# Kernel tuning notes

Hardware: AMD Instinct MI355X
Metric: run time of the kernel (lower is better)

## Reference

```python
import jax, jax.numpy as jnp
import numpy as np

T, H, E, I, K, G, KG = 16384, 1024, 64, 768, 8, 8, 4


def setup_inputs() -> dict:
    key = jax.random.key(0)
    ks = jax.random.split(key, 6)
    return {
        "hidden_states": jax.random.normal(ks[0], (T, H), jnp.float32),
        "gate_weight": jax.random.normal(ks[1], (E, H), jnp.float32) * 0.02,
        "correction_bias": jax.random.normal(ks[2], (E,), jnp.float32) * 0.01,
        "w_gate": jax.random.normal(ks[3], (E, I, H), jnp.float32) * 0.02,
        "w_up": jax.random.normal(ks[4], (E, I, H), jnp.float32) * 0.02,
        "w_down": jax.random.normal(ks[5], (E, H, I), jnp.float32) * 0.02,
    }


def _grouped_topk(hidden, gate_w, bias, top_k=K, n_group=G, topk_group=KG, renormalize=True):
    # gate runs in fp32 (MoEGate.dtype = float32)
    logits = hidden.astype(jnp.float32) @ gate_w.T  # [T, E]
    scores = jax.nn.sigmoid(logits)  # noaux_tc uses sigmoid scores
    s_choice = scores + bias[None, :].astype(jnp.float32)
    t, e = scores.shape
    # group score = sum of top-2 biased scores within each group
    grouped = s_choice.reshape(t, n_group, e // n_group)
    top2, _ = jax.lax.top_k(grouped, 2)
    group_scores = top2.sum(-1)  # [T, G]
    _, gidx = jax.lax.top_k(group_scores, topk_group)  # [T, KG]
    gmask = jnp.zeros((t, n_group), jnp.float32).at[jnp.arange(t)[:, None], gidx].set(1.0)
    emask = jnp.repeat(gmask, e // n_group, axis=1)  # [T, E]
    masked = jnp.where(emask > 0, s_choice, -jnp.inf)
    _, topk_idx = jax.lax.top_k(masked, top_k)  # [T, K]
    # weights use the unbiased sigmoid scores
    topk_w = jnp.take_along_axis(scores, topk_idx, axis=1)
    if renormalize:
        topk_w = topk_w / (topk_w.sum(-1, keepdims=True) + 1e-20)
    # routed_scaling_factor = 1.0
    return topk_idx, topk_w


def reference(hidden_states, gate_weight, correction_bias, w_gate, w_up, w_down):
    t = hidden_states.shape[0]
    topk_idx, topk_w = _grouped_topk(hidden_states, gate_weight, correction_bias)
    # dense combine weights [T, E]: zero except at selected experts
    combine = jnp.zeros((t, E), hidden_states.dtype).at[
        jnp.arange(t)[:, None], topk_idx
    ].add(topk_w.astype(hidden_states.dtype))

    def step(acc, xs):
        wg, wu, wd, c = xs  # wg/wu: [I,H], wd: [H,I], c: [T]
        h = jax.nn.silu(hidden_states @ wg.T) * (hidden_states @ wu.T)  # [T, I]
        return acc + c[:, None] * (h @ wd.T), None

    acc0 = jnp.zeros_like(hidden_states)
    out, _ = jax.lax.scan(step, acc0, (w_gate, w_up, w_down, combine.T))
    return out
```

## Files before the change

### kernel.cpp

```cpp
#include <hip/hip_runtime.h>
#include <hip/hip_bf16.h>
#include <math.h>

#define T_TOK 16384
#define H_DIM 1024
#define E_NUM 64
#define I_DIM 768
#define TOPK  8
#define NGRP  8
#define KGRP  4
#define S_ASN (T_TOK*TOPK)
#define BM 128
#define BK 64
#define MAXBLK (S_ASN/BM + E_NUM)

typedef __attribute__((ext_vector_type(4))) float f4v;
typedef __attribute__((ext_vector_type(8))) short s8v;

#define GLDS16(g, l) __builtin_amdgcn_global_load_lds( \
    (const __attribute__((address_space(1))) void*)(g), \
    (__attribute__((address_space(3))) void*)(l), 16, 0, 0)

static __device__ __forceinline__ short f2bf(float f){
  union { float f; unsigned u; } a; a.f = f;
  unsigned u = a.u;
  unsigned r = (u + 0x7fffu + ((u >> 16) & 1u)) >> 16;
  return (short)r;
}
static __device__ __forceinline__ s8v cvt8(f4v a, f4v b){
  s8v r;
  r[0]=f2bf(a[0]); r[1]=f2bf(a[1]); r[2]=f2bf(a[2]); r[3]=f2bf(a[3]);
  r[4]=f2bf(b[0]); r[5]=f2bf(b[1]); r[6]=f2bf(b[2]); r[7]=f2bf(b[3]);
  return r;
}

__launch_bounds__(256)
__global__ void cast_kernel(const float* __restrict__ src,
                            short* __restrict__ dst, long n8)
{
  long i = (long)blockIdx.x*blockDim.x + threadIdx.x;
  long stride = (long)gridDim.x*blockDim.x;
  for (; i < n8; i += stride){
    f4v a = *(const f4v*)(src + i*8);
    f4v b = *(const f4v*)(src + i*8 + 4);
    *(s8v*)(dst + i*8) = cvt8(a, b);
  }
}

__launch_bounds__(256)
__global__ void gate_kernel(const float* __restrict__ hidden,
                            const float* __restrict__ gate_w,
                            double* __restrict__ logits)
{
  __shared__ float sX[64][33];
  __shared__ float sW[64][33];
  const int tid  = threadIdx.x;
  const int t0   = blockIdx.x * 64;
  const int srow = tid >> 2;
  const int scol = (tid & 3) * 8;
  const int tx = tid & 15, ty = tid >> 4;
  double acc[4][4];
  #pragma unroll
  for (int i=0;i<4;i++)
    #pragma unroll
    for (int j=0;j<4;j++) acc[i][j]=0.0;

  for (int k0=0;k0<H_DIM;k0+=32){
    f4v a0 = *(const f4v*)&hidden[(size_t)(t0+srow)*H_DIM + k0 + scol];
    f4v a1 = *(const f4v*)&hidden[(size_t)(t0+srow)*H_DIM + k0 + scol + 4];
    f4v b0 = *(const f4v*)&gate_w[(size_t)srow*H_DIM + k0 + scol];
    f4v b1 = *(const f4v*)&gate_w[(size_t)srow*H_DIM + k0 + scol + 4];
    __syncthreads();
    #pragma unroll
    for (int j=0;j<4;j++){
      sX[srow][scol+j]   = a0[j];  sX[srow][scol+4+j] = a1[j];
      sW[srow][scol+j]   = b0[j];  sW[srow][scol+4+j] = b1[j];
    }
    __syncthreads();
    #pragma unroll
    for (int kk=0;kk<32;kk++){
      float xv[4], wv[4];
      #pragma unroll
      for (int i=0;i<4;i++){ xv[i]=sX[ty*4+i][kk]; wv[i]=sW[tx*4+i][kk]; }
      #pragma unroll
      for (int i=0;i<4;i++)
        #pragma unroll
        for (int j=0;j<4;j++)
          acc[i][j] += (double)xv[i] * (double)wv[j];
    }
  }
  #pragma unroll
  for (int i=0;i<4;i++)
    #pragma unroll
    for (int j=0;j<4;j++)
      logits[(size_t)(t0+ty*4+i)*E_NUM + tx*4+j] = acc[i][j];
}

__global__ void route_kernel(const double* __restrict__ logits,
                             const float*  __restrict__ bias,
                             int*   __restrict__ topk_idx,
                             float* __restrict__ topk_w,
                             int*   __restrict__ counts)
{
  const int t = blockIdx.x * blockDim.x + threadIdx.x;
  if (t >= T_TOK) return;
  const double* lg = logits + (size_t)t * E_NUM;
  double sc[E_NUM], sch[E_NUM];
  for (int e2=0;e2<E_NUM;e2++){
    double s = 1.0 / (1.0 + exp(-lg[e2]));
    sc[e2]  = s;
    sch[e2] = s + (double)bias[e2];
  }
  double gs[NGRP];
  for (int g=0;g<NGRP;g++){
    double m1=-1e300, m2=-1e300;
    for (int j=0;j<8;j++){
      double v = sch[g*8+j];
      if (v > m1){ m2 = m1; m1 = v; } else if (v > m2){ m2 = v; }
    }
    gs[g] = m1 + m2;
  }
  unsigned gsel = 0;
  for (int r=0;r<KGRP;r++){
    int best = 0; double bv = -1.0e308;
    for (int g=0;g<NGRP;g++)
      if (!((gsel>>g)&1u) && gs[g] > bv){ bv = gs[g]; best = g; }
    gsel |= 1u << best;
  }
  unsigned long long used = 0ULL;
  double wsum = 0.0;
  int sel[TOPK]; double w[TOPK];
  for (int r=0;r<TOPK;r++){
    int best = 0; double bv = -1.0e308;
    for (int e2=0;e2<E_NUM;e2++){
      if ((used>>e2)&1ULL) continue;
      if (!((gsel>>(e2>>3))&1u)) continue;
      if (sch[e2] > bv){ bv = sch[e2]; best = e2; }
    }
    used |= 1ULL << best;
    sel[r] = best;
    w[r]   = sc[best];
    wsum  += w[r];
  }
  double inv = 1.0 / (wsum + 1e-20);
  for (int r=0;r<TOPK;r++){
    topk_idx[(size_t)t*TOPK + r] = sel[r];
    topk_w  [(size_t)t*TOPK + r] = (float)(w[r]*inv);
    atomicAdd(&counts[sel[r]], 1);
  }
}

__global__ void scan_kernel(const int* __restrict__ counts,
                            int* __restrict__ offsets,
                            int* __restrict__ blk_start)
{
  if (threadIdx.x == 0 && blockIdx.x == 0){
    int off = 0, blk = 0;
    for (int e=0;e<E_NUM;e++){
      offsets[e] = off; blk_start[e] = blk;
      off += counts[e];
      blk += (counts[e] + BM - 1) / BM;
    }
    offsets[E_NUM] = off; blk_start[E_NUM] = blk;
  }
}

__global__ void scatter_kernel(const int* __restrict__ topk_idx,
                               const float* __restrict__ topk_w,
                               const int* __restrict__ offsets,
                               int* __restrict__ cursor,
                               int* __restrict__ token_list,
                               float* __restrict__ weight_list)
{
  const int t = blockIdx.x*blockDim.x + threadIdx.x;
  if (t >= T_TOK) return;
  for (int r=0;r<TOPK;r++){
    int   e2 = topk_idx[(size_t)t*TOPK + r];
    float wv = topk_w [(size_t)t*TOPK + r];
    int p = atomicAdd(&cursor[e2], 1);
    token_list [offsets[e2] + p] = t;
    weight_list[offsets[e2] + p] = wv;
  }
}


__launch_bounds__(256, 3)
__global__ void ffn1_fast(const short* __restrict__ hid_bf,
                          const short* __restrict__ wg_bf,
                          const short* __restrict__ wu_bf,
                          const int*   __restrict__ token_list,
                          const float* __restrict__ weight_list,
                          const int*   __restrict__ offsets,
                          const int*   __restrict__ blk_start,
                          short*       __restrict__ h_all)
{
  __shared__ short lsX[128*64];
  __shared__ short lsG[64*64];
  __shared__ short lsU[64*64];
  __shared__ float lsWt[128];

  const int bx = blockIdx.x;
  if (bx >= blk_start[E_NUM]) return;
  int e = 0;
  while (blk_start[e+1] <= bx) ++e;
  const int rb   = bx - blk_start[e];
  const int cb   = blockIdx.y;
  const int base = offsets[e];
  const int n_e  = offsets[e+1] - base;
  const int row0 = rb * BM;

  const int tid = threadIdx.x;
  const int lane = tid & 63, wid = tid >> 6;
  const int wm = wid >> 1, wn = wid & 1;
  const int l15 = lane & 15, l4 = lane >> 4;

  if (tid < BM) lsWt[tid] = ((row0+tid) < n_e) ? weight_list[base+row0+tid] : 0.f;

  const short* srcA[4];
  #pragma unroll
  for (int i=0;i<4;i++){
    int s_lin = i*256 + tid;
    int row = s_lin >> 3, sl = s_lin & 7;
    int asn = base + row0 + row; if (asn >= S_ASN) asn = S_ASN-1;
    int tok = token_list[asn];
    srcA[i] = hid_bf + (size_t)tok*H_DIM + ((sl ^ (row&7))<<3);
  }
  const short* srcG[2]; const short* srcU[2];
  #pragma unroll
  for (int i=0;i<2;i++){
    int s_lin = i*256 + tid;
    int row = s_lin >> 3, sl = s_lin & 7;
    size_t wrow = ((size_t)e*I_DIM + cb*64 + row)*H_DIM + ((sl ^ (row&7))<<3);
    srcG[i] = wg_bf + wrow;
    srcU[i] = wu_bf + wrow;
  }
  short* dstA0 = lsX + wid*512;
  short* dstG0 = lsG + wid*512;
  short* dstU0 = lsU + wid*512;

  f4v accg[4][2], accu[4][2];
  #pragma unroll
  for (int m=0;m<4;m++)
    #pragma unroll
    for (int n=0;n<2;n++){
      accg[m][n]=(f4v){0.f,0.f,0.f,0.f};
      accu[m][n]=(f4v){0.f,0.f,0.f,0.f};
    }

  for (int k0=0; k0<H_DIM; k0+=BK){
    __syncthreads();
    #pragma unroll
    for (int i=0;i<4;i++) GLDS16(srcA[i]+k0, dstA0 + i*2048);
    #pragma unroll
    for (int i=0;i<2;i++) GLDS16(srcG[i]+k0, dstG0 + i*2048);
    #pragma unroll
    for (int i=0;i<2;i++) GLDS16(srcU[i]+k0, dstU0 + i*2048);
    __syncthreads();
    #pragma unroll
    for (int kk=0;kk<2;kk++){
      s8v af[4], bg[2], bu[2];
      #pragma unroll
      for (int m=0;m<4;m++){
        int r = wm*64 + m*16 + l15;
        int s = (kk*4 + l4) ^ (r & 7);
        af[m] = *(const s8v*)&lsX[r*64 + (s<<3)];
      }
      #pragma unroll
      for (int n=0;n<2;n++){
        int r = wn*32 + n*16 + l15;
        int s = (kk*4 + l4) ^ (r & 7);
        bg[n] = *(const s8v*)&lsG[r*64 + (s<<3)];
        bu[n] = *(const s8v*)&lsU[r*64 + (s<<3)];
      }
      #pragma unroll
      for (int m=0;m<4;m++)
        #pragma unroll
        for (int n=0;n<2;n++){
          accg[m][n] = __builtin_amdgcn_mfma_f32_16x16x32_bf16(af[m], bg[n], accg[m][n], 0,0,0);
          accu[m][n] = __builtin_amdgcn_mfma_f32_16x16x32_bf16(af[m], bu[n], accu[m][n], 0,0,0);
        }
    }
  }
  #pragma unroll
  for (int m=0;m<4;m++){
    #pragma unroll
    for (int i=0;i<4;i++){
      int r = wm*64 + m*16 + l4*4 + i;
      if (row0 + r < n_e){
        float wgt = lsWt[r];
        size_t hb = (size_t)(base+row0+r)*I_DIM + (size_t)cb*64;
        #pragma unroll
        for (int n=0;n<2;n++){
          int c = wn*32 + n*16 + l15;
          float g = accg[m][n][i], u = accu[m][n][i];
          float s = g / (1.f + __expf(-g));
          h_all[hb + c] = f2bf(s * u * wgt);
        }
      }
    }
  }
}

__launch_bounds__(256, 3)
__global__ void ffn2_fast(const short* __restrict__ h_all,
                          const short* __restrict__ wd_bf,
                          const int*   __restrict__ token_list,
                          const int*   __restrict__ offsets,
                          const int*   __restrict__ blk_start,
                          float*       __restrict__ out)
{
  __shared__ short lsA[128*64];
  __shared__ short lsB[128*64];
  __shared__ int   lsT[128];

  const int bx = blockIdx.x;
  if (bx >= blk_start[E_NUM]) return;
  int e = 0;
  while (blk_start[e+1] <= bx) ++e;
  const int rb   = bx - blk_start[e];
  const int cb   = blockIdx.y;
  const int base = offsets[e];
  const int n_e  = offsets[e+1] - base;
  const int row0 = rb * BM;

  const int tid = threadIdx.x;
  const int lane = tid & 63, wid = tid >> 6;
  const int wm = wid >> 1, wn = wid & 1;
  const int l15 = lane & 15, l4 = lane >> 4;

  if (tid < BM) lsT[tid] = ((row0+tid) < n_e) ? token_list[base+row0+tid] : -1;

  const short* srcA[4]; const short* srcB[4];
  #pragma unroll
  for (int i=0;i<4;i++){
    int s_lin = i*256 + tid;
    int row = s_lin >> 3, sl = s_lin & 7;
    int arow = base + row0 + row; if (arow >= S_ASN) arow = S_ASN-1;
    srcA[i] = h_all + (size_t)arow*I_DIM + ((sl ^ (row&7))<<3);
    srcB[i] = wd_bf + ((size_t)e*H_DIM + cb*128 + row)*I_DIM + ((sl ^ (row&7))<<3);
  }
  short* dstA0 = lsA + wid*512;
  short* dstB0 = lsB + wid*512;

  f4v acc[4][4];
  #pragma unroll
  for (int m=0;m<4;m++)
    #pragma unroll
    for (int n=0;n<4;n++) acc[m][n]=(f4v){0.f,0.f,0.f,0.f};

  for (int k0=0; k0<I_DIM; k0+=BK){
    __syncthreads();
    #pragma unroll
    for (int i=0;i<4;i++) GLDS16(srcA[i]+k0, dstA0 + i*2048);
    #pragma unroll
    for (int i=0;i<4;i++) GLDS16(srcB[i]+k0, dstB0 + i*2048);
    __syncthreads();
    #pragma unroll
    for (int kk=0;kk<2;kk++){
      s8v af[4], bf[4];
      #pragma unroll
      for (int m=0;m<4;m++){
        int r = wm*64 + m*16 + l15;
        int s = (kk*4 + l4) ^ (r & 7);
        af[m] = *(const s8v*)&lsA[r*64 + (s<<3)];
      }
      #pragma unroll
      for (int n=0;n<4;n++){
        int r = wn*64 + n*16 + l15;
        int s = (kk*4 + l4) ^ (r & 7);
        bf[n] = *(const s8v*)&lsB[r*64 + (s<<3)];
      }
      #pragma unroll
      for (int m=0;m<4;m++)
        #pragma unroll
        for (int n=0;n<4;n++)
          acc[m][n] = __builtin_amdgcn_mfma_f32_16x16x32_bf16(af[m], bf[n], acc[m][n], 0,0,0);
    }
  }
  #pragma unroll
  for (int m=0;m<4;m++){
    #pragma unroll
    for (int i=0;i<4;i++){
      int r = wm*64 + m*16 + l4*4 + i;
      int tk = lsT[r];
      if (tk >= 0){
        #pragma unroll
        for (int n=0;n<4;n++){
          int c = cb*128 + wn*64 + n*16 + l15;
          atomicAdd(&out[(size_t)tk*H_DIM + c], acc[m][n][i]);
        }
      }
    }
  }
}

__launch_bounds__(512, 2)
__global__ void ffn1_kernel(const float* __restrict__ hidden,
                            const float* __restrict__ w_gate,
                            const float* __restrict__ w_up,
                            const int*   __restrict__ token_list,
                            const float* __restrict__ weight_list,
                            const int*   __restrict__ offsets,
                            const int*   __restrict__ blk_start,
                            short*       __restrict__ h_all)
{
  __shared__ short lsX[BM*64];
  __shared__ short lsG[BM*64];
  __shared__ short lsU[BM*64];
  __shared__ float lsWt[BM];

  const int bx = blockIdx.x;
  if (bx >= blk_start[E_NUM]) return;
  int e = 0;
  while (blk_start[e+1] <= bx) ++e;
  const int rb   = bx - blk_start[e];
  const int cb   = blockIdx.y;
  const int base = offsets[e];
  const int n_e  = offsets[e+1] - base;
  const int row0 = rb * BM;

  const int tid   = threadIdx.x;
  const int srow  = tid >> 2;
  const int scol  = (tid & 3) << 4;
  const int slot0 = (tid & 3) << 1;
  const int wsl0  = srow*64 + (((slot0  ) ^ (srow & 7)) << 3);
  const int wsl1  = srow*64 + (((slot0+1) ^ (srow & 7)) << 3);

  const bool tvalid = (row0 + srow) < n_e;
  int tok = 0;
  if (tvalid) tok = token_list[base + row0 + srow];
  const float* xsrc = hidden + (size_t)tok * H_DIM + scol;
  const size_t woff = (size_t)e * I_DIM * H_DIM + (size_t)(cb*128 + srow) * H_DIM + scol;
  const float* gsrc = w_gate + woff;
  const float* usrc = w_up   + woff;

  const int lane = tid & 63, wid = tid >> 6;
  const int wm = wid >> 2, wn = wid & 3;
  const int l15 = lane & 15, l4 = lane >> 4;

  f4v accg[4][2], accu[4][2];
  #pragma unroll
  for (int m=0;m<4;m++)
    #pragma unroll
    for (int n=0;n<2;n++){
      accg[m][n]=(f4v){0.f,0.f,0.f,0.f};
      accu[m][n]=(f4v){0.f,0.f,0.f,0.f};
    }

  for (int k0=0; k0<H_DIM; k0+=BK){
    f4v x0,x1,x2,x3;
    if (tvalid){
      x0 = *(const f4v*)(xsrc+k0);   x1 = *(const f4v*)(xsrc+k0+4);
      x2 = *(const f4v*)(xsrc+k0+8); x3 = *(const f4v*)(xsrc+k0+12);
    } else {
      x0=x1=x2=x3=(f4v){0.f,0.f,0.f,0.f};
    }
    f4v g0 = *(const f4v*)(gsrc+k0),   g1 = *(const f4v*)(gsrc+k0+4);
    f4v g2 = *(const f4v*)(gsrc+k0+8), g3 = *(const f4v*)(gsrc+k0+12);
    f4v u0 = *(const f4v*)(usrc+k0),   u1 = *(const f4v*)(usrc+k0+4);
    f4v u2 = *(const f4v*)(usrc+k0+8), u3 = *(const f4v*)(usrc+k0+12);
    __syncthreads();
    *(s8v*)&lsX[wsl0] = cvt8(x0,x1);  *(s8v*)&lsX[wsl1] = cvt8(x2,x3);
    *(s8v*)&lsG[wsl0] = cvt8(g0,g1);  *(s8v*)&lsG[wsl1] = cvt8(g2,g3);
    *(s8v*)&lsU[wsl0] = cvt8(u0,u1);  *(s8v*)&lsU[wsl1] = cvt8(u2,u3);
    __syncthreads();
    #pragma unroll
    for (int kk=0;kk<2;kk++){
      s8v af[4], bg[2], bu[2];
      #pragma unroll
      for (int m=0;m<4;m++){
        int r = wm*64 + m*16 + l15;
        int s = (kk*4 + l4) ^ (r & 7);
        af[m] = *(const s8v*)&lsX[r*64 + (s<<3)];
      }
      #pragma unroll
      for (int n=0;n<2;n++){
        int r = wn*32 + n*16 + l15;
        int s = (kk*4 + l4) ^ (r & 7);
        bg[n] = *(const s8v*)&lsG[r*64 + (s<<3)];
        bu[n] = *(const s8v*)&lsU[r*64 + (s<<3)];
      }
      #pragma unroll
      for (int m=0;m<4;m++)
        #pragma unroll
        for (int n=0;n<2;n++){
          accg[m][n] = __builtin_amdgcn_mfma_f32_16x16x32_bf16(af[m], bg[n], accg[m][n], 0,0,0);
          accu[m][n] = __builtin_amdgcn_mfma_f32_16x16x32_bf16(af[m], bu[n], accu[m][n], 0,0,0);
        }
    }
  }
  if (tid < BM) lsWt[tid] = ((row0+tid) < n_e) ? weight_list[base+row0+tid] : 0.f;
  __syncthreads();
  #pragma unroll
  for (int m=0;m<4;m++){
    #pragma unroll
    for (int i=0;i<4;i++){
      int r = wm*64 + m*16 + l4*4 + i;
      if (row0 + r < n_e){
        float wgt = lsWt[r];
        size_t hb = (size_t)(base+row0+r)*I_DIM + (size_t)cb*128;
        #pragma unroll
        for (int n=0;n<2;n++){
          int c = wn*32 + n*16 + l15;
          float g = accg[m][n][i], u = accu[m][n][i];
          float s = g / (1.f + __expf(-g));
          h_all[hb + c] = f2bf(s * u * wgt);
        }
      }
    }
  }
}

__launch_bounds__(512, 2)
__global__ void ffn2_kernel(const short* __restrict__ h_all,
                            const float* __restrict__ w_down,
                            const int*   __restrict__ token_list,
                            const int*   __restrict__ offsets,
                            const int*   __restrict__ blk_start,
                            float*       __restrict__ out)
{
  __shared__ short lsA[BM*64];
  __shared__ short lsB[BM*64];
  __shared__ int   lsT[BM];

  const int bx = blockIdx.x;
  if (bx >= blk_start[E_NUM]) return;
  int e = 0;
  while (blk_start[e+1] <= bx) ++e;
  const int rb   = bx - blk_start[e];
  const int cb   = blockIdx.y;
  const int base = offsets[e];
  const int n_e  = offsets[e+1] - base;
  const int row0 = rb * BM;

  const int tid   = threadIdx.x;
  const int srow  = tid >> 2;
  const int slot0 = (tid & 3) << 1;
  const int wsl0  = srow*64 + (((slot0  ) ^ (srow & 7)) << 3);
  const int wsl1  = srow*64 + (((slot0+1) ^ (srow & 7)) << 3);

  int arow = base + row0 + srow;
  if (arow >= S_ASN) arow = S_ASN - 1;
  const short* asrc = h_all + (size_t)arow*I_DIM + ((tid&3)<<4);
  const float* bsrc = w_down + (size_t)e*H_DIM*I_DIM
                    + (size_t)(cb*128 + srow)*I_DIM + ((tid&3)<<4);

  const int lane = tid & 63, wid = tid >> 6;
  const int wm = wid >> 2, wn = wid & 3;
  const int l15 = lane & 15, l4 = lane >> 4;

  f4v acc[4][2];
  #pragma unroll
  for (int m=0;m<4;m++)
    #pragma unroll
    for (int n=0;n<2;n++) acc[m][n]=(f4v){0.f,0.f,0.f,0.f};

  for (int k0=0; k0<I_DIM; k0+=BK){
    s8v alo = *(const s8v*)(asrc + k0);
    s8v ahi = *(const s8v*)(asrc + k0 + 8);
    f4v b0 = *(const f4v*)(bsrc+k0),   b1 = *(const f4v*)(bsrc+k0+4);
    f4v b2 = *(const f4v*)(bsrc+k0+8), b3 = *(const f4v*)(bsrc+k0+12);
    __syncthreads();
    *(s8v*)&lsA[wsl0] = alo;          *(s8v*)&lsA[wsl1] = ahi;
    *(s8v*)&lsB[wsl0] = cvt8(b0,b1);  *(s8v*)&lsB[wsl1] = cvt8(b2,b3);
    __syncthreads();
    #pragma unroll
    for (int kk=0;kk<2;kk++){
      s8v af[4], bf[2];
      #pragma unroll
      for (int m=0;m<4;m++){
        int r = wm*64 + m*16 + l15;
        int s = (kk*4 + l4) ^ (r & 7);
        af[m] = *(const s8v*)&lsA[r*64 + (s<<3)];
      }
      #pragma unroll
      for (int n=0;n<2;n++){
        int r = wn*32 + n*16 + l15;
        int s = (kk*4 + l4) ^ (r & 7);
        bf[n] = *(const s8v*)&lsB[r*64 + (s<<3)];
      }
      #pragma unroll
      for (int m=0;m<4;m++)
        #pragma unroll
        for (int n=0;n<2;n++)
          acc[m][n] = __builtin_amdgcn_mfma_f32_16x16x32_bf16(af[m], bf[n], acc[m][n], 0,0,0);
    }
  }
  if (tid < BM) lsT[tid] = ((row0+tid) < n_e) ? token_list[base+row0+tid] : -1;
  __syncthreads();
  #pragma unroll
  for (int m=0;m<4;m++){
    #pragma unroll
    for (int i=0;i<4;i++){
      int r = wm*64 + m*16 + l4*4 + i;
      int tk = lsT[r];
      if (tk >= 0){
        #pragma unroll
        for (int n=0;n<2;n++){
          int c = cb*128 + wn*32 + n*16 + l15;
          atomicAdd(&out[(size_t)tk*H_DIM + c], acc[m][n][i]);
        }
      }
    }
  }
}

extern "C" void kernel_launch(void* const* d_in, const int* in_sizes, int n_in,
                              void* d_out, int out_size, void* d_ws, size_t ws_size,
                              hipStream_t stream)
{
  const float* hidden = (const float*)d_in[0];
  const float* gate_w = (const float*)d_in[1];
  const float* bias   = (const float*)d_in[2];
  const float* w_gate = (const float*)d_in[3];
  const float* w_up   = (const float*)d_in[4];
  const float* w_down = (const float*)d_in[5];
  float* out = (float*)d_out;

  char* ws = (char*)d_ws;
  size_t off = 0;
  #define WALLOC(bytes) (ws + off); off += (((size_t)(bytes)) + 255) & ~(size_t)255
  double* logits    = (double*)WALLOC((size_t)T_TOK*E_NUM*8);
  int*    topk_idx  = (int*)   WALLOC((size_t)T_TOK*TOPK*4);
  float*  topk_w    = (float*) WALLOC((size_t)T_TOK*TOPK*4);
  int*    counts    = (int*)   WALLOC(256);
  int*    cursor    = (int*)   WALLOC(256);
  int*    offsets   = (int*)   WALLOC(512);
  int*    blk_st    = (int*)   WALLOC(512);
  int*    token_l   = (int*)   WALLOC((size_t)S_ASN*4);
  float*  weight_l  = (float*) WALLOC((size_t)S_ASN*4);
  short*  h_all     = (short*) WALLOC((size_t)S_ASN*I_DIM*2);
  const size_t base_need = off;
  short*  hid_bf    = (short*) WALLOC((size_t)T_TOK*H_DIM*2);
  short*  wg_bf     = (short*) WALLOC((size_t)E_NUM*I_DIM*H_DIM*2);
  short*  wu_bf     = (short*) WALLOC((size_t)E_NUM*I_DIM*H_DIM*2);
  short*  wd_bf     = (short*) WALLOC((size_t)E_NUM*H_DIM*I_DIM*2);
  const size_t fast_need = off;
  #undef WALLOC

  const bool fast = (ws_size >= fast_need);
  if (ws_size < base_need) return;

  hipMemsetAsync(counts, 0, 512, stream);
  hipMemsetAsync(out, 0, (size_t)T_TOK*H_DIM*4, stream);

  gate_kernel   <<<T_TOK/64,  256, 0, stream>>>(hidden, gate_w, logits);
  route_kernel  <<<T_TOK/256, 256, 0, stream>>>(logits, bias, topk_idx, topk_w, counts);
  scan_kernel   <<<1, 64, 0, stream>>>(counts, offsets, blk_st);
  scatter_kernel<<<T_TOK/256, 256, 0, stream>>>(topk_idx, topk_w, offsets, cursor,
                                                token_l, weight_l);
  if (fast){
    long n8h = (long)T_TOK*H_DIM/8;
    long n8w = (long)E_NUM*I_DIM*H_DIM/8;
    cast_kernel<<<2048, 256, 0, stream>>>(hidden, hid_bf, n8h);
    cast_kernel<<<2048, 256, 0, stream>>>(w_gate, wg_bf, n8w);
    cast_kernel<<<2048, 256, 0, stream>>>(w_up,   wu_bf, n8w);
    cast_kernel<<<2048, 256, 0, stream>>>(w_down, wd_bf, n8w);
    dim3 g1(MAXBLK, I_DIM/64);
    ffn1_fast<<<g1, 256, 0, stream>>>(hid_bf, wg_bf, wu_bf, token_l, weight_l,
                                      offsets, blk_st, h_all);
    dim3 g2(MAXBLK, H_DIM/128);
    ffn2_fast<<<g2, 256, 0, stream>>>(h_all, wd_bf, token_l, offsets, blk_st, out);
  } else {
    dim3 g1(MAXBLK, I_DIM/128);
    ffn1_kernel<<<g1, 512, 0, stream>>>(hidden, w_gate, w_up, token_l, weight_l,
                                        offsets, blk_st, h_all);
    dim3 g2(MAXBLK, H_DIM/128);
    ffn2_kernel<<<g2, 512, 0, stream>>>(h_all, w_down, token_l, offsets, blk_st, out);
  }
}
```

Baseline: 1.923 ms.

## Pin experts to XCDs with per-XCD work tables and grid-stride tile loops

Builds per-XCD work tables in which each expert's tiles all go to one XCD (expert e maps to XCD e&7), filled by a new fill_kernel from offsets computed in the scan. The FFN kernels now launch a fixed grid and stride over their XCD's table, so the blocks that share an expert's weights run on the same XCD and reuse them through its L2. The aim is to cut repeated weight fetches from HBM. Launch bounds also go from 3 to 4 blocks per CU. The risks are load imbalance across XCDs when expert counts are uneven, and the assumption that blocks are dealt to XCDs round-robin by blockIdx.

```diff
diff --git a/kernel.cpp b/kernel.cpp
--- a/kernel.cpp
+++ b/kernel.cpp
@@ -13,6 +13,10 @@
 #define BM 128
 #define BK 64
 #define MAXBLK (S_ASN/BM + E_NUM)
+#define NCB1 (I_DIM/64)
+#define NCB2 (H_DIM/128)
+#define XCAP 16384
+#define XSTRIDE 2048
 
 typedef __attribute__((ext_vector_type(4))) float f4v;
 typedef __attribute__((ext_vector_type(8))) short s8v;
@@ -152,17 +156,42 @@
 
 __global__ void scan_kernel(const int* __restrict__ counts,
                             int* __restrict__ offsets,
-                            int* __restrict__ blk_start)
+                            int* __restrict__ blk_start,
+                            int* __restrict__ xoff,
+                            int* __restrict__ qblk)
 {
   if (threadIdx.x == 0 && blockIdx.x == 0){
     int off = 0, blk = 0;
+    int cnt[8];
+    for (int x=0;x<8;x++) cnt[x]=0;
     for (int e=0;e<E_NUM;e++){
       offsets[e] = off; blk_start[e] = blk;
+      int nblk = (counts[e] + BM - 1) / BM;
+      xoff[e] = cnt[e & 7];
+      cnt[e & 7] += nblk;
       off += counts[e];
-      blk += (counts[e] + BM - 1) / BM;
+      blk += nblk;
     }
     offsets[E_NUM] = off; blk_start[E_NUM] = blk;
-  }
+    for (int x=0;x<8;x++) qblk[x] = cnt[x];
+  }
+}
+
+__global__ void fill_kernel(const int* __restrict__ offsets,
+                            const int* __restrict__ xoff,
+                            int* __restrict__ tab1,
+                            int* __restrict__ tab2)
+{
+  const int e = blockIdx.x;
+  const int n_e  = offsets[e+1] - offsets[e];
+  const int nblk = (n_e + BM - 1) / BM;
+  const int x = e & 7;
+  int* t1 = tab1 + (size_t)x*XCAP + xoff[e]*NCB1;
+  int* t2 = tab2 + (size_t)x*XCAP + xoff[e]*NCB2;
+  for (int i = threadIdx.x; i < nblk*NCB1; i += blockDim.x)
+    t1[i] = (e<<18) | ((i/NCB1)<<4) | (i%NCB1);
+  for (int i = threadIdx.x; i < nblk*NCB2; i += blockDim.x)
+    t2[i] = (e<<18) | ((i/NCB2)<<4) | (i%NCB2);
 }
 
 __global__ void scatter_kernel(const int* __restrict__ topk_idx,
@@ -184,14 +213,15 @@
 }
 
 
-__launch_bounds__(256, 3)
+__launch_bounds__(256, 4)
 __global__ void ffn1_fast(const short* __restrict__ hid_bf,
                           const short* __restrict__ wg_bf,
                           const short* __restrict__ wu_bf,
                           const int*   __restrict__ token_list,
                           const float* __restrict__ weight_list,
                           const int*   __restrict__ offsets,
-                          const int*   __restrict__ blk_start,
+                          const int*   __restrict__ tab1,
+                          const int*   __restrict__ qblk,
                           short*       __restrict__ h_all)
 {
   __shared__ short lsX[128*64];
@@ -199,195 +229,204 @@
   __shared__ short lsU[64*64];
   __shared__ float lsWt[128];
 
-  const int bx = blockIdx.x;
-  if (bx >= blk_start[E_NUM]) return;
-  int e = 0;
-  while (blk_start[e+1] <= bx) ++e;
-  const int rb   = bx - blk_start[e];
-  const int cb   = blockIdx.y;
-  const int base = offsets[e];
-  const int n_e  = offsets[e+1] - base;
-  const int row0 = rb * BM;
-
+  const int xcd = blockIdx.x & 7;
+  const int q0  = blockIdx.x >> 3;
+  const int qn  = qblk[xcd] * NCB1;
   const int tid = threadIdx.x;
   const int lane = tid & 63, wid = tid >> 6;
   const int wm = wid >> 1, wn = wid & 1;
   const int l15 = lane & 15, l4 = lane >> 4;
 
-  if (tid < BM) lsWt[tid] = ((row0+tid) < n_e) ? weight_list[base+row0+tid] : 0.f;
-
-  const short* srcA[4];
-  #pragma unroll
-  for (int i=0;i<4;i++){
-    int s_lin = i*256 + tid;
-    int row = s_lin >> 3, sl = s_lin & 7;
-    int asn = base + row0 + row; if (asn >= S_ASN) asn = S_ASN-1;
-    int tok = token_list[asn];
-    srcA[i] = hid_bf + (size_t)tok*H_DIM + ((sl ^ (row&7))<<3);
-  }
-  const short* srcG[2]; const short* srcU[2];
-  #pragma unroll
-  for (int i=0;i<2;i++){
-    int s_lin = i*256 + tid;
-    int row = s_lin >> 3, sl = s_lin & 7;
-    size_t wrow = ((size_t)e*I_DIM + cb*64 + row)*H_DIM + ((sl ^ (row&7))<<3);
-    srcG[i] = wg_bf + wrow;
-    srcU[i] = wu_bf + wrow;
-  }
-  short* dstA0 = lsX + wid*512;
-  short* dstG0 = lsG + wid*512;
-  short* dstU0 = lsU + wid*512;
-
-  f4v accg[4][2], accu[4][2];
-  #pragma unroll
-  for (int m=0;m<4;m++)
-    #pragma unroll
-    for (int n=0;n<2;n++){
-      accg[m][n]=(f4v){0.f,0.f,0.f,0.f};
-      accu[m][n]=(f4v){0.f,0.f,0.f,0.f};
-    }
-
-  for (int k0=0; k0<H_DIM; k0+=BK){
+  for (int q = q0; q < qn; q += XSTRIDE){
+    const int v  = tab1[(size_t)xcd*XCAP + q];
+    const int e  = v >> 18;
+    const int rb = (v >> 4) & 16383;
+    const int cb = v & 15;
+    const int base = offsets[e];
+    const int n_e  = offsets[e+1] - base;
+    const int row0 = rb * BM;
+
     __syncthreads();
-    #pragma unroll
-    for (int i=0;i<4;i++) GLDS16(srcA[i]+k0, dstA0 + i*2048);
-    #pragma unroll
-    for (int i=0;i<2;i++) GLDS16(srcG[i]+k0, dstG0 + i*2048);
-    #pragma unroll
-    for (int i=0;i<2;i++) GLDS16(srcU[i]+k0, dstU0 + i*2048);
-    __syncthreads();
-    #pragma unroll
-    for (int kk=0;kk<2;kk++){
-      s8v af[4], bg[2], bu[2];
-      #pragma unroll
-      for (int m=0;m<4;m++){
-        int r = wm*64 + m*16 + l15;
-        int s = (kk*4 + l4) ^ (r & 7);
-        af[m] = *(const s8v*)&lsX[r*64 + (s<<3)];
-      }
+    if (tid < BM) lsWt[tid] = ((row0+tid) < n_e) ? weight_list[base+row0+tid] : 0.f;
+
+    const short* srcA[4];
+    #pragma unroll
+    for (int i=0;i<4;i++){
+      int s_lin = i*256 + tid;
+      int row = s_lin >> 3, sl = s_lin & 7;
+      int asn = base + row0 + row; if (asn >= S_ASN) asn = S_ASN-1;
+      int tok = token_list[asn];
+      srcA[i] = hid_bf + (size_t)tok*H_DIM + ((sl ^ (row&7))<<3);
+    }
+    const short* srcG[2]; const short* srcU[2];
+    #pragma unroll
+    for (int i=0;i<2;i++){
+      int s_lin = i*256 + tid;
+      int row = s_lin >> 3, sl = s_lin & 7;
+      size_t wrow = ((size_t)e*I_DIM + cb*64 + row)*H_DIM + ((sl ^ (row&7))<<3);
+      srcG[i] = wg_bf + wrow;
+      srcU[i] = wu_bf + wrow;
+    }
+    short* dstA0 = lsX + wid*512;
+    short* dstG0 = lsG + wid*512;
+    short* dstU0 = lsU + wid*512;
+
+    f4v accg[4][2], accu[4][2];
+    #pragma unroll
+    for (int m=0;m<4;m++)
       #pragma unroll
       for (int n=0;n<2;n++){
-        int r = wn*32 + n*16 + l15;
-        int s = (kk*4 + l4) ^ (r & 7);
-        bg[n] = *(const s8v*)&lsG[r*64 + (s<<3)];
-        bu[n] = *(const s8v*)&lsU[r*64 + (s<<3)];
-      }
-      #pragma unroll
-      for (int m=0;m<4;m++)
+        accg[m][n]=(f4v){0.f,0.f,0.f,0.f};
+        accu[m][n]=(f4v){0.f,0.f,0.f,0.f};
+      }
+
+    for (int k0=0; k0<H_DIM; k0+=BK){
+      __syncthreads();
+      #pragma unroll
+      for (int i=0;i<4;i++) GLDS16(srcA[i]+k0, dstA0 + i*2048);
+      #pragma unroll
+      for (int i=0;i<2;i++) GLDS16(srcG[i]+k0, dstG0 + i*2048);
+      #pragma unroll
+      for (int i=0;i<2;i++) GLDS16(srcU[i]+k0, dstU0 + i*2048);
+      __syncthreads();
+      #pragma unroll
+      for (int kk=0;kk<2;kk++){
+        s8v af[4], bg[2], bu[2];
+        #pragma unroll
+        for (int m=0;m<4;m++){
+          int r = wm*64 + m*16 + l15;
+          int s = (kk*4 + l4) ^ (r & 7);
+          af[m] = *(const s8v*)&lsX[r*64 + (s<<3)];
+        }
         #pragma unroll
         for (int n=0;n<2;n++){
-          accg[m][n] = __builtin_amdgcn_mfma_f32_16x16x32_bf16(af[m], bg[n], accg[m][n], 0,0,0);
-          accu[m][n] = __builtin_amdgcn_mfma_f32_16x16x32_bf16(af[m], bu[n], accu[m][n], 0,0,0);
-        }
-    }
-  }
-  #pragma unroll
-  for (int m=0;m<4;m++){
-    #pragma unroll
-    for (int i=0;i<4;i++){
-      int r = wm*64 + m*16 + l4*4 + i;
-      if (row0 + r < n_e){
-        float wgt = lsWt[r];
-        size_t hb = (size_t)(base+row0+r)*I_DIM + (size_t)cb*64;
-        #pragma unroll
-        for (int n=0;n<2;n++){
-          int c = wn*32 + n*16 + l15;
-          float g = accg[m][n][i], u = accu[m][n][i];
-          float s = g / (1.f + __expf(-g));
-          h_all[hb + c] = f2bf(s * u * wgt);
-        }
-      }
-    }
-  }
-}
-
-__launch_bounds__(256, 3)
+          int r = wn*32 + n*16 + l15;
+          int s = (kk*4 + l4) ^ (r & 7);
+          bg[n] = *(const s8v*)&lsG[r*64 + (s<<3)];
+          bu[n] = *(const s8v*)&lsU[r*64 + (s<<3)];
+        }
+        #pragma unroll
+        for (int m=0;m<4;m++)
+          #pragma unroll
+          for (int n=0;n<2;n++){
+            accg[m][n] = __builtin_amdgcn_mfma_f32_16x16x32_bf16(af[m], bg[n], accg[m][n], 0,0,0);
+            accu[m][n] = __builtin_amdgcn_mfma_f32_16x16x32_bf16(af[m], bu[n], accu[m][n], 0,0,0);
+          }
+      }
+    }
+    #pragma unroll
+    for (int m=0;m<4;m++){
+      #pragma unroll
+      for (int i=0;i<4;i++){
+        int r = wm*64 + m*16 + l4*4 + i;
+        if (row0 + r < n_e){
+          float wgt = lsWt[r];
+          size_t hb = (size_t)(base+row0+r)*I_DIM + (size_t)cb*64;
+          #pragma unroll
+          for (int n=0;n<2;n++){
+            int c = wn*32 + n*16 + l15;
+            float g = accg[m][n][i], u = accu[m][n][i];
+            float s = g / (1.f + __expf(-g));
+            h_all[hb + c] = f2bf(s * u * wgt);
+          }
+        }
+      }
+    }
+  }
+}
+
+__launch_bounds__(256, 4)
 __global__ void ffn2_fast(const short* __restrict__ h_all,
                           const short* __restrict__ wd_bf,
                           const int*   __restrict__ token_list,
                           const int*   __restrict__ offsets,
-                          const int*   __restrict__ blk_start,
+                          const int*   __restrict__ tab2,
+                          const int*   __restrict__ qblk,
                           float*       __restrict__ out)
 {
   __shared__ short lsA[128*64];
   __shared__ short lsB[128*64];
   __shared__ int   lsT[128];
 
-  const int bx = blockIdx.x;
-  if (bx >= blk_start[E_NUM]) return;
-  int e = 0;
-  while (blk_start[e+1] <= bx) ++e;
-  const int rb   = bx - blk_start[e];
-  const int cb   = blockIdx.y;
-  const int base = offsets[e];
-  const int n_e  = offsets[e+1] - base;
-  const int row0 = rb * BM;
-
+  const int xcd = blockIdx.x & 7;
+  const int q0  = blockIdx.x >> 3;
+  const int qn  = qblk[xcd] * NCB2;
   const int tid = threadIdx.x;
   const int lane = tid & 63, wid = tid >> 6;
   const int wm = wid >> 1, wn = wid & 1;
   const int l15 = lane & 15, l4 = lane >> 4;
 
-  if (tid < BM) lsT[tid] = ((row0+tid) < n_e) ? token_list[base+row0+tid] : -1;
-
-  const short* srcA[4]; const short* srcB[4];
-  #pragma unroll
-  for (int i=0;i<4;i++){
-    int s_lin = i*256 + tid;
-    int row = s_lin >> 3, sl = s_lin & 7;
-    int arow = base + row0 + row; if (arow >= S_ASN) arow = S_ASN-1;
-    srcA[i] = h_all + (size_t)arow*I_DIM + ((sl ^ (row&7))<<3);
-    srcB[i] = wd_bf + ((size_t)e*H_DIM + cb*128 + row)*I_DIM + ((sl ^ (row&7))<<3);
-  }
-  short* dstA0 = lsA + wid*512;
-  short* dstB0 = lsB + wid*512;
-
-  f4v acc[4][4];
-  #pragma unroll
-  for (int m=0;m<4;m++)
-    #pragma unroll
-    for (int n=0;n<4;n++) acc[m][n]=(f4v){0.f,0.f,0.f,0.f};
-
-  for (int k0=0; k0<I_DIM; k0+=BK){
+  for (int q = q0; q < qn; q += XSTRIDE){
+    const int v  = tab2[(size_t)xcd*XCAP + q];
+    const int e  = v >> 18;
+    const int rb = (v >> 4) & 16383;
+    const int cb = v & 15;
+    const int base = offsets[e];
+    const int n_e  = offsets[e+1] - base;
+    const int row0 = rb * BM;
+
     __syncthreads();
-    #pragma unroll
-    for (int i=0;i<4;i++) GLDS16(srcA[i]+k0, dstA0 + i*2048);
-    #pragma unroll
-    for (int i=0;i<4;i++) GLDS16(srcB[i]+k0, dstB0 + i*2048);
-    __syncthreads();
-    #pragma unroll
-    for (int kk=0;kk<2;kk++){
-      s8v af[4], bf[4];
-      #pragma unroll
-      for (int m=0;m<4;m++){
-        int r = wm*64 + m*16 + l15;
-        int s = (kk*4 + l4) ^ (r & 7);
-        af[m] = *(const s8v*)&lsA[r*64 + (s<<3)];
-      }
-      #pragma unroll
-      for (int n=0;n<4;n++){
-        int r = wn*64 + n*16 + l15;
-        int s = (kk*4 + l4) ^ (r & 7);
-        bf[n] = *(const s8v*)&lsB[r*64 + (s<<3)];
-      }
-      #pragma unroll
-      for (int m=0;m<4;m++)
-        #pragma unroll
-        for (int n=0;n<4;n++)
-          acc[m][n] = __builtin_amdgcn_mfma_f32_16x16x32_bf16(af[m], bf[n], acc[m][n], 0,0,0);
-    }
-  }
-  #pragma unroll
-  for (int m=0;m<4;m++){
+    if (tid < BM) lsT[tid] = ((row0+tid) < n_e) ? token_list[base+row0+tid] : -1;
+
+    const short* srcA[4]; const short* srcB[4];
     #pragma unroll
     for (int i=0;i<4;i++){
-      int r = wm*64 + m*16 + l4*4 + i;
-      int tk = lsT[r];
-      if (tk >= 0){
+      int s_lin = i*256 + tid;
+      int row = s_lin >> 3, sl = s_lin & 7;
+      int arow = base + row0 + row; if (arow >= S_ASN) arow = S_ASN-1;
+      srcA[i] = h_all + (size_t)arow*I_DIM + ((sl ^ (row&7))<<3);
+      srcB[i] = wd_bf + ((size_t)e*H_DIM + cb*128 + row)*I_DIM + ((sl ^ (row&7))<<3);
+    }
+    short* dstA0 = lsA + wid*512;
+    short* dstB0 = lsB + wid*512;
+
+    f4v acc[4][4];
+    #pragma unroll
+    for (int m=0;m<4;m++)
+      #pragma unroll
+      for (int n=0;n<4;n++) acc[m][n]=(f4v){0.f,0.f,0.f,0.f};
+
+    for (int k0=0; k0<I_DIM; k0+=BK){
+      __syncthreads();
+      #pragma unroll
+      for (int i=0;i<4;i++) GLDS16(srcA[i]+k0, dstA0 + i*2048);
+      #pragma unroll
+      for (int i=0;i<4;i++) GLDS16(srcB[i]+k0, dstB0 + i*2048);
+      __syncthreads();
+      #pragma unroll
+      for (int kk=0;kk<2;kk++){
+        s8v af[4], bf[4];
+        #pragma unroll
+        for (int m=0;m<4;m++){
+          int r = wm*64 + m*16 + l15;
+          int s = (kk*4 + l4) ^ (r & 7);
+          af[m] = *(const s8v*)&lsA[r*64 + (s<<3)];
+        }
         #pragma unroll
         for (int n=0;n<4;n++){
-          int c = cb*128 + wn*64 + n*16 + l15;
-          atomicAdd(&out[(size_t)tk*H_DIM + c], acc[m][n][i]);
+          int r = wn*64 + n*16 + l15;
+          int s = (kk*4 + l4) ^ (r & 7);
+          bf[n] = *(const s8v*)&lsB[r*64 + (s<<3)];
+        }
+        #pragma unroll
+        for (int m=0;m<4;m++)
+          #pragma unroll
+          for (int n=0;n<4;n++)
+            acc[m][n] = __builtin_amdgcn_mfma_f32_16x16x32_bf16(af[m], bf[n], acc[m][n], 0,0,0);
+      }
+    }
+    #pragma unroll
+    for (int m=0;m<4;m++){
+      #pragma unroll
+      for (int i=0;i<4;i++){
+        int r = wm*64 + m*16 + l4*4 + i;
+        int tk = lsT[r];
+        if (tk >= 0){
+          #pragma unroll
+          for (int n=0;n<4;n++){
+            int c = cb*128 + wn*64 + n*16 + l15;
+            atomicAdd(&out[(size_t)tk*H_DIM + c], acc[m][n][i]);
+          }
         }
       }
     }
@@ -627,10 +666,14 @@
   int*    cursor    = (int*)   WALLOC(256);
   int*    offsets   = (int*)   WALLOC(512);
   int*    blk_st    = (int*)   WALLOC(512);
+  int*    xoff      = (int*)   WALLOC(256);
+  int*    qblk      = (int*)   WALLOC(256);
   int*    token_l   = (int*)   WALLOC((size_t)S_ASN*4);
   float*  weight_l  = (float*) WALLOC((size_t)S_ASN*4);
   short*  h_all     = (short*) WALLOC((size_t)S_ASN*I_DIM*2);
   const size_t base_need = off;
+  int*    tab1      = (int*)   WALLOC((size_t)8*XCAP*4);
+  int*    tab2      = (int*)   WALLOC((size_t)8*XCAP*4);
   short*  hid_bf    = (short*) WALLOC((size_t)T_TOK*H_DIM*2);
   short*  wg_bf     = (short*) WALLOC((size_t)E_NUM*I_DIM*H_DIM*2);
   short*  wu_bf     = (short*) WALLOC((size_t)E_NUM*I_DIM*H_DIM*2);
@@ -646,7 +689,7 @@
 
   gate_kernel   <<<T_TOK/64,  256, 0, stream>>>(hidden, gate_w, logits);
   route_kernel  <<<T_TOK/256, 256, 0, stream>>>(logits, bias, topk_idx, topk_w, counts);
-  scan_kernel   <<<1, 64, 0, stream>>>(counts, offsets, blk_st);
+  scan_kernel   <<<1, 64, 0, stream>>>(counts, offsets, blk_st, xoff, qblk);
   scatter_kernel<<<T_TOK/256, 256, 0, stream>>>(topk_idx, topk_w, offsets, cursor,
                                                 token_l, weight_l);
   if (fast){
@@ -656,11 +699,11 @@
     cast_kernel<<<2048, 256, 0, stream>>>(w_gate, wg_bf, n8w);
     cast_kernel<<<2048, 256, 0, stream>>>(w_up,   wu_bf, n8w);
     cast_kernel<<<2048, 256, 0, stream>>>(w_down, wd_bf, n8w);
-    dim3 g1(MAXBLK, I_DIM/64);
-    ffn1_fast<<<g1, 256, 0, stream>>>(hid_bf, wg_bf, wu_bf, token_l, weight_l,
-                                      offsets, blk_st, h_all);
-    dim3 g2(MAXBLK, H_DIM/128);
-    ffn2_fast<<<g2, 256, 0, stream>>>(h_all, wd_bf, token_l, offsets, blk_st, out);
+    fill_kernel<<<E_NUM, 256, 0, stream>>>(offsets, xoff, tab1, tab2);
+    ffn1_fast<<<8*XSTRIDE, 256, 0, stream>>>(hid_bf, wg_bf, wu_bf, token_l, weight_l,
+                                             offsets, tab1, qblk, h_all);
+    ffn2_fast<<<8*XSTRIDE, 256, 0, stream>>>(h_all, wd_bf, token_l,
+                                             offsets, tab2, qblk, out);
   } else {
     dim3 g1(MAXBLK, I_DIM/128);
     ffn1_kernel<<<g1, 512, 0, stream>>>(hidden, w_gate, w_up, token_l, weight_l,
```

Measured after the change: 2.396 ms. +24.6%, slower.
